# Optimization experiments

Measured on AMD Instinct MI355X. Metric: run time of the kernel, lower is better.

The kernel has to match this reference:

```python
import jax, jax.numpy as jnp
import numpy as np

B, S, H = 4, 2048, 2048
FFN, E, TOP_K = 5632, 8, 2

def setup_inputs() -> dict:
    key = jax.random.key(0)
    k1, k2, k3, k4, k5 = jax.random.split(key, 5)
    return {
        "hidden_states": jax.random.normal(k1, (B, S, H), dtype=jnp.float32),
        "wg": jax.random.normal(k2, (H, E), dtype=jnp.float32) * 0.02,
        "wg_ema": jnp.zeros((H, E), dtype=jnp.float32),
        "fc1_1": jax.random.normal(k3, (E, FFN, H), dtype=jnp.float32) * 0.02,
        "fc1_2": jax.random.normal(k4, (E, FFN, H), dtype=jnp.float32) * 0.02,
        "fc2": jax.random.normal(k5, (E, H, FFN), dtype=jnp.float32) * 0.02,
    }

def reference(hidden_states, wg, wg_ema, fc1_1, fc1_2, fc2):
    b, s, h = hidden_states.shape
    x = hidden_states.reshape(-1, h)  # [T, H]
    # Router: P6TopkCapGate mixes the live gate with its EMA 50/50.
    wg_running = 0.5 * (wg_ema + wg.astype(jnp.float32))
    router_logits = x.astype(jnp.float32) @ wg_running  # [T, E]
    probs = jax.nn.softmax(router_logits, axis=-1)
    top_vals, top_idx = jax.lax.top_k(probs, TOP_K)  # [T, K]
    routing_weights = (top_vals / top_vals.sum(axis=-1, keepdims=True)).astype(x.dtype)
    out = jnp.zeros_like(x)
    n_experts = fc1_1.shape[0]
    for e in range(n_experts):
        # combine weight per token for this expert (0 if not routed here)
        w_e = jnp.sum(routing_weights * (top_idx == e), axis=-1)  # [T]
        h1 = x @ fc1_1[e].T            # [T, FFN]
        h2 = x @ fc1_2[e].T            # [T, FFN]
        y = (jax.nn.silu(h1) * h2) @ fc2[e].T  # [T, H]
        out = out + w_e[:, None] * y
    return out.reshape(b, s, h), router_logits
```

## Files before the change

### kernel.cpp

```cpp
#include <hip/hip_runtime.h>
#include <stdint.h>

#define TT 8192
#define HD 2048
#define FFN 5632
#define NE 8
#define NPK 11264

typedef float f32x4 __attribute__((ext_vector_type(4)));
typedef _Float16 f16x8 __attribute__((ext_vector_type(8)));
typedef unsigned int u32;

#define OFF_WR    0ul
#define OFF_CNT   65536ul
#define OFF_LISTS 66048ul
#define OFF_TOKW  328192ul
#define OFF_ACT   1048576ul
#define OFF_XH    (OFF_ACT + 184549376ul)
#define OFF_WPK   (OFF_XH + 33554432ul)
#define OFF_W3H   OFF_WPK

__device__ __forceinline__ void gl_lds16(const void* g, void* s) {
  __builtin_amdgcn_global_load_lds((const __attribute__((address_space(1))) u32*)g,
                                   (__attribute__((address_space(3))) u32*)s, 16, 0, 0);
}

__device__ __forceinline__ f16x8 cvt8(f32x4 a, f32x4 b) {
  f16x8 r;
  r[0] = (_Float16)a[0]; r[1] = (_Float16)a[1]; r[2] = (_Float16)a[2]; r[3] = (_Float16)a[3];
  r[4] = (_Float16)b[0]; r[5] = (_Float16)b[1]; r[6] = (_Float16)b[2]; r[7] = (_Float16)b[3];
  return r;
}

__global__ __launch_bounds__(256) void k_cvt(const float* __restrict__ in,
                                             _Float16* __restrict__ out, long n8) {
  long i = (long)blockIdx.x * 256 + threadIdx.x;
  const long stride = (long)gridDim.x * 256;
  for (; i < n8; i += stride) {
    f32x4 a = ((const f32x4*)in)[i * 2];
    f32x4 b = ((const f32x4*)in)[i * 2 + 1];
    ((f16x8*)out)[i] = cvt8(a, b);
  }
}

__global__ __launch_bounds__(256) void k_cvtpack(const float* __restrict__ fc11,
                                                 const float* __restrict__ fc12,
                                                 _Float16* __restrict__ wpk) {
  const long total = (long)NE * NPK * 256;
  long i8 = (long)blockIdx.x * 256 + threadIdx.x;
  const long stride = (long)gridDim.x * 256;
  for (; i8 < total; i8 += stride) {
    int k8 = (int)(i8 & 255);
    long qe = i8 >> 8;
    int q = (int)(qe % NPK);
    int e = (int)(qe / NPK);
    int c = q & 127;
    int f = (q >> 7) * 64 + ((c >> 6) & 1) * 32 + ((c >> 4) & 1) * 16 + (c & 15);
    const float* src = ((c >> 5) & 1 ? fc12 : fc11) + ((size_t)e * FFN + f) * HD + k8 * 8;
    f32x4 a = *(const f32x4*)src;
    f32x4 b = *(const f32x4*)(src + 4);
    *(f16x8*)(wpk + qe * HD + (size_t)k8 * 8) = cvt8(a, b);
  }
}

__global__ __launch_bounds__(256) void k_prep(const float* __restrict__ wg,
                                              const float* __restrict__ wge,
                                              float* __restrict__ wr) {
  int i = blockIdx.x * 256 + threadIdx.x;
  if (i < HD * NE) wr[i] = 0.5f * (wge[i] + wg[i]);
}

__global__ __launch_bounds__(256) void k_router(const float* __restrict__ x,
                                                const float* __restrict__ wr,
                                                float* __restrict__ logits,
                                                float* __restrict__ tokw,
                                                int* __restrict__ lists,
                                                int* __restrict__ cnt) {
  const int t = blockIdx.x, tid = threadIdx.x;
  const float* xr = x + (size_t)t * HD;
  float acc[NE];
#pragma unroll
  for (int e = 0; e < NE; ++e) acc[e] = 0.f;
  for (int h = tid; h < HD; h += 256) {
    float xv = xr[h];
    const float* w = wr + h * NE;
#pragma unroll
    for (int e = 0; e < NE; ++e) acc[e] = fmaf(xv, w[e], acc[e]);
  }
#pragma unroll
  for (int e = 0; e < NE; ++e)
#pragma unroll
    for (int off = 32; off; off >>= 1)
      acc[e] += __shfl_xor(acc[e], off, 64);
  __shared__ float red[4][NE];
  int wv = tid >> 6;
  if ((tid & 63) == 0)
    for (int e = 0; e < NE; ++e) red[wv][e] = acc[e];
  __syncthreads();
  if (tid == 0) {
    float l[NE];
#pragma unroll
    for (int e = 0; e < NE; ++e) l[e] = red[0][e] + red[1][e] + red[2][e] + red[3][e];
#pragma unroll
    for (int e = 0; e < NE; ++e) logits[(size_t)t * NE + e] = l[e];
    int i0 = 0;
    for (int e = 1; e < NE; ++e) if (l[e] > l[i0]) i0 = e;
    int i1 = -1;
    for (int e = 0; e < NE; ++e) if (e != i0 && (i1 < 0 || l[e] > l[i1])) i1 = e;
    float p1 = __expf(l[i1] - l[i0]);
    float s = 1.f + p1;
    tokw[t * 2]     = 1.f / s;
    tokw[t * 2 + 1] = p1 / s;
    int q0 = atomicAdd(&cnt[i0], 1);
    lists[i0 * TT + q0] = t * 2;
    int q1 = atomicAdd(&cnt[i1], 1);
    lists[i1 * TT + q1] = t * 2 + 1;
  }
}

__global__ __launch_bounds__(256, 3) void k_ffn1(const _Float16* __restrict__ xh,
                                                 const _Float16* __restrict__ wpk,
                                                 const int* __restrict__ lists,
                                                 const int* __restrict__ cnt,
                                                 _Float16* __restrict__ act) {
  const int bid = blockIdx.x;
  const int xk = bid & 7;
  const int sq = bid >> 3;
  const int slot = sq / 352;
  const int within = sq - slot * 352;
  const int ct = within >> 2;
  const int rt_in = within & 3;
  const int e = slot & 7;
  const int r = ((xk - e) & 7) + ((slot >> 3) << 3);
  const int rt = r * 4 + rt_in;
  const int count = cnt[e];
  if (rt * 128 >= count) return;
  const int tid = threadIdx.x, lane = tid & 63, wv = tid >> 6;

  __shared__ __align__(16) _Float16 As[2][4096];
  __shared__ __align__(16) _Float16 Bs[2][4096];
  __shared__ int row_pair[128];

  if (tid < 128) {
    int rg = rt * 128 + tid;
    row_pair[tid] = (rg < count) ? lists[e * TT + rg] : -1;
  }
  __syncthreads();

  const int lr = lane >> 2;
  const int srow = wv * 32 + lr;
  const int cp = (lane & 3) ^ ((srow >> 1) & 3);
  const int p0 = row_pair[srow], p1 = row_pair[srow + 16];
  const _Float16* gA0 = xh + (size_t)(p0 >= 0 ? (p0 >> 1) : 0) * HD + cp * 8;
  const _Float16* gA1 = xh + (size_t)(p1 >= 0 ? (p1 >> 1) : 0) * HD + cp * 8;
  const _Float16* gB0 = wpk + ((size_t)e * NPK + (size_t)ct * 128 + srow) * HD + cp * 8;
  const _Float16* gB1 = gB0 + (size_t)16 * HD;

  auto stage = [&](int sl, int k0) {
    gl_lds16(gA0 + k0, &As[sl][wv * 1024]);
    gl_lds16(gA1 + k0, &As[sl][wv * 1024 + 512]);
    gl_lds16(gB0 + k0, &Bs[sl][wv * 1024]);
    gl_lds16(gB1 + k0, &Bs[sl][wv * 1024 + 512]);
  };

  const f32x4 z4 = {0.f, 0.f, 0.f, 0.f};
  f32x4 acc[4][4];
#pragma unroll
  for (int m = 0; m < 4; ++m)
#pragma unroll
    for (int n = 0; n < 4; ++n) acc[m][n] = z4;

  const int fr = lane & 15, kq = lane >> 4;
  const int wrow = (wv >> 1) * 64, wcol = (wv & 1) * 64;
  int aoff[4], boff[4];
#pragma unroll
  for (int m = 0; m < 4; ++m) {
    int rr = wrow + m * 16 + fr;
    aoff[m] = rr * 32 + (kq ^ ((rr >> 1) & 3)) * 8;
  }
#pragma unroll
  for (int n = 0; n < 4; ++n) {
    int rr = wcol + n * 16 + fr;
    boff[n] = rr * 32 + (kq ^ ((rr >> 1) & 3)) * 8;
  }

  stage(0, 0);
  __syncthreads();

  const int NS = HD / 32;
  for (int ks = 0; ks < NS; ++ks) {
    const int buf = ks & 1;
    if (ks + 1 < NS) stage(buf ^ 1, (ks + 1) * 32);
    f16x8 fa[4], fb[4];
#pragma unroll
    for (int m = 0; m < 4; ++m) fa[m] = *(const f16x8*)&As[buf][aoff[m]];
#pragma unroll
    for (int n = 0; n < 4; ++n) fb[n] = *(const f16x8*)&Bs[buf][boff[n]];
    __builtin_amdgcn_s_setprio(1);
#pragma unroll
    for (int m = 0; m < 4; ++m)
#pragma unroll
      for (int n = 0; n < 4; ++n)
        acc[m][n] = __builtin_amdgcn_mfma_f32_16x16x32_f16(fa[m], fb[n], acc[m][n], 0, 0, 0);
    __builtin_amdgcn_s_setprio(0);
    __syncthreads();
  }

  const int wn = wv & 1;
  const int rbase = wrow + kq * 4;
#pragma unroll
  for (int m = 0; m < 4; ++m) {
#pragma unroll
    for (int n = 0; n < 2; ++n) {
      const int f = ct * 64 + wn * 32 + n * 16 + fr;
#pragma unroll
      for (int j = 0; j < 4; ++j) {
        int rl = rbase + m * 16 + j;
        int pr = row_pair[rl];
        if (pr >= 0) {
          float h1 = acc[m][n][j], h2 = acc[m][n + 2][j];
          float sv = h1 / (1.f + __expf(-h1));
          act[(size_t)pr * FFN + f] = (_Float16)(sv * h2);
        }
      }
    }
  }
}

__global__ __launch_bounds__(256, 3) void k_ffn2(const _Float16* __restrict__ act,
                                                 const _Float16* __restrict__ w3h,
                                                 const int* __restrict__ lists,
                                                 const int* __restrict__ cnt,
                                                 const float* __restrict__ tokw,
                                                 float* __restrict__ out) {
  const int bid = blockIdx.x;
  const int xk = bid & 7;
  const int sq = bid >> 3;
  const int e = sq >> 7;
  const int within = sq & 127;
  const int rt = within >> 1;
  const int ct = (((xk - e) & 7) << 1) + (within & 1);
  const int count = cnt[e];
  if (rt * 128 >= count) return;
  const int tid = threadIdx.x, lane = tid & 63, wv = tid >> 6;

  __shared__ __align__(16) _Float16 As[2][4096];
  __shared__ __align__(16) _Float16 Bs[2][4096];
  __shared__ int row_pair[128];
  __shared__ float row_w[128];

  if (tid < 128) {
    int rg = rt * 128 + tid;
    int pr = (rg < count) ? lists[e * TT + rg] : -1;
    row_pair[tid] = pr;
    row_w[tid] = (pr >= 0) ? tokw[pr] : 0.f;
  }
  __syncthreads();

  const int lr = lane >> 2;
  const int srow = wv * 32 + lr;
  const int cp = (lane & 3) ^ ((srow >> 1) & 3);
  const int p0 = row_pair[srow], p1 = row_pair[srow + 16];
  const _Float16* gA0 = act + (size_t)(p0 >= 0 ? p0 : 0) * FFN + cp * 8;
  const _Float16* gA1 = act + (size_t)(p1 >= 0 ? p1 : 0) * FFN + cp * 8;
  const _Float16* gB0 = w3h + ((size_t)e * HD + (size_t)ct * 128 + srow) * FFN + cp * 8;
  const _Float16* gB1 = gB0 + (size_t)16 * FFN;

  auto stage = [&](int sl, int k0) {
    gl_lds16(gA0 + k0, &As[sl][wv * 1024]);
    gl_lds16(gA1 + k0, &As[sl][wv * 1024 + 512]);
    gl_lds16(gB0 + k0, &Bs[sl][wv * 1024]);
    gl_lds16(gB1 + k0, &Bs[sl][wv * 1024 + 512]);
  };

  const f32x4 z4 = {0.f, 0.f, 0.f, 0.f};
  f32x4 acc[4][4];
#pragma unroll
  for (int m = 0; m < 4; ++m)
#pragma unroll
    for (int n = 0; n < 4; ++n) acc[m][n] = z4;

  const int fr = lane & 15, kq = lane >> 4;
  const int wrow = (wv >> 1) * 64, wcol = (wv & 1) * 64;
  int aoff[4], boff[4];
#pragma unroll
  for (int m = 0; m < 4; ++m) {
    int rr = wrow + m * 16 + fr;
    aoff[m] = rr * 32 + (kq ^ ((rr >> 1) & 3)) * 8;
  }
#pragma unroll
  for (int n = 0; n < 4; ++n) {
    int rr = wcol + n * 16 + fr;
    boff[n] = rr * 32 + (kq ^ ((rr >> 1) & 3)) * 8;
  }

  stage(0, 0);
  __syncthreads();

  const int NS = FFN / 32;
  for (int ks = 0; ks < NS; ++ks) {
    const int buf = ks & 1;
    if (ks + 1 < NS) stage(buf ^ 1, (ks + 1) * 32);
    f16x8 fa[4], fb[4];
#pragma unroll
    for (int m = 0; m < 4; ++m) fa[m] = *(const f16x8*)&As[buf][aoff[m]];
#pragma unroll
    for (int n = 0; n < 4; ++n) fb[n] = *(const f16x8*)&Bs[buf][boff[n]];
    __builtin_amdgcn_s_setprio(1);
#pragma unroll
    for (int m = 0; m < 4; ++m)
#pragma unroll
      for (int n = 0; n < 4; ++n)
        acc[m][n] = __builtin_amdgcn_mfma_f32_16x16x32_f16(fa[m], fb[n], acc[m][n], 0, 0, 0);
    __builtin_amdgcn_s_setprio(0);
    __syncthreads();
  }

  const int rbase = wrow + kq * 4;
#pragma unroll
  for (int m = 0; m < 4; ++m) {
#pragma unroll
    for (int n = 0; n < 4; ++n) {
      const int col = ct * 128 + wcol + n * 16 + fr;
#pragma unroll
      for (int j = 0; j < 4; ++j) {
        int rl = rbase + m * 16 + j;
        int pr = row_pair[rl];
        if (pr >= 0) {
          float v = acc[m][n][j] * row_w[rl];
          unsafeAtomicAdd(out + (size_t)(pr >> 1) * HD + col, v);
        }
      }
    }
  }
}

extern "C" void kernel_launch(void* const* d_in, const int* in_sizes, int n_in,
                              void* d_out, int out_size, void* d_ws, size_t ws_size,
                              hipStream_t stream) {
  (void)in_sizes; (void)n_in; (void)out_size; (void)ws_size;
  const float* x    = (const float*)d_in[0];
  const float* wg   = (const float*)d_in[1];
  const float* wge  = (const float*)d_in[2];
  const float* fc11 = (const float*)d_in[3];
  const float* fc12 = (const float*)d_in[4];
  const float* fc2  = (const float*)d_in[5];
  float* out    = (float*)d_out;
  float* logits = out + (size_t)TT * HD;

  char* ws = (char*)d_ws;
  float* wr      = (float*)(ws + OFF_WR);
  int*   cnt     = (int*)(ws + OFF_CNT);
  int*   lists   = (int*)(ws + OFF_LISTS);
  float* tokw    = (float*)(ws + OFF_TOKW);
  _Float16* act  = (_Float16*)(ws + OFF_ACT);
  _Float16* xh   = (_Float16*)(ws + OFF_XH);
  _Float16* wpk  = (_Float16*)(ws + OFF_WPK);
  _Float16* w3h  = (_Float16*)(ws + OFF_W3H);

  hipMemsetAsync(out, 0, (size_t)TT * HD * sizeof(float), stream);
  hipMemsetAsync(cnt, 0, NE * sizeof(int), stream);

  k_prep<<<dim3((HD * NE + 255) / 256), 256, 0, stream>>>(wg, wge, wr);
  k_router<<<dim3(TT), 256, 0, stream>>>(x, wr, logits, tokw, lists, cnt);

  k_cvt<<<dim3(2048), 256, 0, stream>>>(x, xh, (long)TT * HD / 8);
  k_cvtpack<<<dim3(2048), 256, 0, stream>>>(fc11, fc12, wpk);

  k_ffn1<<<dim3(64 * 88 * NE), 256, 0, stream>>>(xh, wpk, lists, cnt, act);

  k_cvt<<<dim3(2048), 256, 0, stream>>>(fc2, w3h, (long)NE * HD * FFN / 8);

  k_ffn2<<<dim3(64 * 16 * NE), 256, 0, stream>>>(act, w3h, lists, cnt, tokw, out);
}
```

Measured before the change: 2.193 ms.

## Switch expert GEMMs to 32x32x16 MFMA and fuse x fp16 conversion into router

Both expert GEMM kernels now use 32x32x16 f16 MFMA tiles with 16-wide accumulators in place of 16x16x32 tiles. The LDS fragment offsets, the packed weight interleave, and the epilogue row mapping are rewritten to match the new output layout. The router kernel now also writes the fp16 copy of x, which removes the separate conversion kernel and its extra pass over x. Larger MFMA tiles issue fewer instructions and need fewer LDS fragment reads per FLOP, at the cost of different register pressure and a more intricate epilogue layout.

```diff
diff --git a/kernel.cpp b/kernel.cpp
--- a/kernel.cpp
+++ b/kernel.cpp
@@ -8,6 +8,7 @@
 #define NPK 11264
 
 typedef float f32x4 __attribute__((ext_vector_type(4)));
+typedef float f32x16 __attribute__((ext_vector_type(16)));
 typedef _Float16 f16x8 __attribute__((ext_vector_type(8)));
 typedef unsigned int u32;
 
@@ -55,7 +56,7 @@
     int q = (int)(qe % NPK);
     int e = (int)(qe / NPK);
     int c = q & 127;
-    int f = (q >> 7) * 64 + ((c >> 6) & 1) * 32 + ((c >> 4) & 1) * 16 + (c & 15);
+    int f = (q >> 7) * 64 + ((c >> 6) & 1) * 32 + (c & 31);
     const float* src = ((c >> 5) & 1 ? fc12 : fc11) + ((size_t)e * FFN + f) * HD + k8 * 8;
     f32x4 a = *(const f32x4*)src;
     f32x4 b = *(const f32x4*)(src + 4);
@@ -75,14 +76,17 @@
                                                 float* __restrict__ logits,
                                                 float* __restrict__ tokw,
                                                 int* __restrict__ lists,
-                                                int* __restrict__ cnt) {
+                                                int* __restrict__ cnt,
+                                                _Float16* __restrict__ xh) {
   const int t = blockIdx.x, tid = threadIdx.x;
   const float* xr = x + (size_t)t * HD;
+  _Float16* xo = xh + (size_t)t * HD;
   float acc[NE];
 #pragma unroll
   for (int e = 0; e < NE; ++e) acc[e] = 0.f;
   for (int h = tid; h < HD; h += 256) {
     float xv = xr[h];
+    xo[h] = (_Float16)xv;
     const float* w = wr + h * NE;
 #pragma unroll
     for (int e = 0; e < NE; ++e) acc[e] = fmaf(xv, w[e], acc[e]);
@@ -163,25 +167,32 @@
     gl_lds16(gB1 + k0, &Bs[sl][wv * 1024 + 512]);
   };
 
-  const f32x4 z4 = {0.f, 0.f, 0.f, 0.f};
-  f32x4 acc[4][4];
-#pragma unroll
-  for (int m = 0; m < 4; ++m)
-#pragma unroll
-    for (int n = 0; n < 4; ++n) acc[m][n] = z4;
-
-  const int fr = lane & 15, kq = lane >> 4;
+  f32x16 acc[2][2];
+#pragma unroll
+  for (int mi = 0; mi < 2; ++mi)
+#pragma unroll
+    for (int ni = 0; ni < 2; ++ni) acc[mi][ni] = (f32x16)0.f;
+
+  const int l31 = lane & 31, kq5 = lane >> 5;
   const int wrow = (wv >> 1) * 64, wcol = (wv & 1) * 64;
-  int aoff[4], boff[4];
-#pragma unroll
-  for (int m = 0; m < 4; ++m) {
-    int rr = wrow + m * 16 + fr;
-    aoff[m] = rr * 32 + (kq ^ ((rr >> 1) & 3)) * 8;
-  }
-#pragma unroll
-  for (int n = 0; n < 4; ++n) {
-    int rr = wcol + n * 16 + fr;
-    boff[n] = rr * 32 + (kq ^ ((rr >> 1) & 3)) * 8;
+  int aoff[2][2], boff[2][2];
+#pragma unroll
+  for (int mi = 0; mi < 2; ++mi) {
+    int row = wrow + mi * 32 + l31;
+#pragma unroll
+    for (int kb = 0; kb < 2; ++kb) {
+      int gi = kb * 2 + kq5;
+      aoff[mi][kb] = row * 32 + ((gi ^ ((row >> 1) & 3)) << 3);
+    }
+  }
+#pragma unroll
+  for (int ni = 0; ni < 2; ++ni) {
+    int row = wcol + ni * 32 + l31;
+#pragma unroll
+    for (int kb = 0; kb < 2; ++kb) {
+      int gi = kb * 2 + kq5;
+      boff[ni][kb] = row * 32 + ((gi ^ ((row >> 1) & 3)) << 3);
+    }
   }
 
   stage(0, 0);
@@ -191,37 +202,39 @@
   for (int ks = 0; ks < NS; ++ks) {
     const int buf = ks & 1;
     if (ks + 1 < NS) stage(buf ^ 1, (ks + 1) * 32);
-    f16x8 fa[4], fb[4];
-#pragma unroll
-    for (int m = 0; m < 4; ++m) fa[m] = *(const f16x8*)&As[buf][aoff[m]];
-#pragma unroll
-    for (int n = 0; n < 4; ++n) fb[n] = *(const f16x8*)&Bs[buf][boff[n]];
+    f16x8 fa[2][2], fb[2][2];
+#pragma unroll
+    for (int mi = 0; mi < 2; ++mi)
+#pragma unroll
+      for (int kb = 0; kb < 2; ++kb) fa[mi][kb] = *(const f16x8*)&As[buf][aoff[mi][kb]];
+#pragma unroll
+    for (int ni = 0; ni < 2; ++ni)
+#pragma unroll
+      for (int kb = 0; kb < 2; ++kb) fb[ni][kb] = *(const f16x8*)&Bs[buf][boff[ni][kb]];
     __builtin_amdgcn_s_setprio(1);
 #pragma unroll
-    for (int m = 0; m < 4; ++m)
-#pragma unroll
-      for (int n = 0; n < 4; ++n)
-        acc[m][n] = __builtin_amdgcn_mfma_f32_16x16x32_f16(fa[m], fb[n], acc[m][n], 0, 0, 0);
+    for (int kb = 0; kb < 2; ++kb)
+#pragma unroll
+      for (int mi = 0; mi < 2; ++mi)
+#pragma unroll
+        for (int ni = 0; ni < 2; ++ni)
+          acc[mi][ni] = __builtin_amdgcn_mfma_f32_32x32x16_f16(fa[mi][kb], fb[ni][kb], acc[mi][ni], 0, 0, 0);
     __builtin_amdgcn_s_setprio(0);
     __syncthreads();
   }
 
   const int wn = wv & 1;
-  const int rbase = wrow + kq * 4;
-#pragma unroll
-  for (int m = 0; m < 4; ++m) {
-#pragma unroll
-    for (int n = 0; n < 2; ++n) {
-      const int f = ct * 64 + wn * 32 + n * 16 + fr;
-#pragma unroll
-      for (int j = 0; j < 4; ++j) {
-        int rl = rbase + m * 16 + j;
-        int pr = row_pair[rl];
-        if (pr >= 0) {
-          float h1 = acc[m][n][j], h2 = acc[m][n + 2][j];
-          float sv = h1 / (1.f + __expf(-h1));
-          act[(size_t)pr * FFN + f] = (_Float16)(sv * h2);
-        }
+  const int f = ct * 64 + wn * 32 + l31;
+#pragma unroll
+  for (int mi = 0; mi < 2; ++mi) {
+#pragma unroll
+    for (int rr = 0; rr < 16; ++rr) {
+      int row = wrow + mi * 32 + (rr & 3) + 8 * (rr >> 2) + 4 * kq5;
+      int pr = row_pair[row];
+      if (pr >= 0) {
+        float h1 = acc[mi][0][rr], h2 = acc[mi][1][rr];
+        float sv = h1 / (1.f + __expf(-h1));
+        act[(size_t)pr * FFN + f] = (_Float16)(sv * h2);
       }
     }
   }
@@ -273,25 +286,32 @@
     gl_lds16(gB1 + k0, &Bs[sl][wv * 1024 + 512]);
   };
 
-  const f32x4 z4 = {0.f, 0.f, 0.f, 0.f};
-  f32x4 acc[4][4];
-#pragma unroll
-  for (int m = 0; m < 4; ++m)
-#pragma unroll
-    for (int n = 0; n < 4; ++n) acc[m][n] = z4;
-
-  const int fr = lane & 15, kq = lane >> 4;
+  f32x16 acc[2][2];
+#pragma unroll
+  for (int mi = 0; mi < 2; ++mi)
+#pragma unroll
+    for (int ni = 0; ni < 2; ++ni) acc[mi][ni] = (f32x16)0.f;
+
+  const int l31 = lane & 31, kq5 = lane >> 5;
   const int wrow = (wv >> 1) * 64, wcol = (wv & 1) * 64;
-  int aoff[4], boff[4];
-#pragma unroll
-  for (int m = 0; m < 4; ++m) {
-    int rr = wrow + m * 16 + fr;
-    aoff[m] = rr * 32 + (kq ^ ((rr >> 1) & 3)) * 8;
-  }
-#pragma unroll
-  for (int n = 0; n < 4; ++n) {
-    int rr = wcol + n * 16 + fr;
-    boff[n] = rr * 32 + (kq ^ ((rr >> 1) & 3)) * 8;
+  int aoff[2][2], boff[2][2];
+#pragma unroll
+  for (int mi = 0; mi < 2; ++mi) {
+    int row = wrow + mi * 32 + l31;
+#pragma unroll
+    for (int kb = 0; kb < 2; ++kb) {
+      int gi = kb * 2 + kq5;
+      aoff[mi][kb] = row * 32 + ((gi ^ ((row >> 1) & 3)) << 3);
+    }
+  }
+#pragma unroll
+  for (int ni = 0; ni < 2; ++ni) {
+    int row = wcol + ni * 32 + l31;
+#pragma unroll
+    for (int kb = 0; kb < 2; ++kb) {
+      int gi = kb * 2 + kq5;
+      boff[ni][kb] = row * 32 + ((gi ^ ((row >> 1) & 3)) << 3);
+    }
   }
 
   stage(0, 0);
@@ -301,33 +321,38 @@
   for (int ks = 0; ks < NS; ++ks) {
     const int buf = ks & 1;
     if (ks + 1 < NS) stage(buf ^ 1, (ks + 1) * 32);
-    f16x8 fa[4], fb[4];
-#pragma unroll
-    for (int m = 0; m < 4; ++m) fa[m] = *(const f16x8*)&As[buf][aoff[m]];
-#pragma unroll
-    for (int n = 0; n < 4; ++n) fb[n] = *(const f16x8*)&Bs[buf][boff[n]];
+    f16x8 fa[2][2], fb[2][2];
+#pragma unroll
+    for (int mi = 0; mi < 2; ++mi)
+#pragma unroll
+      for (int kb = 0; kb < 2; ++kb) fa[mi][kb] = *(const f16x8*)&As[buf][aoff[mi][kb]];
+#pragma unroll
+    for (int ni = 0; ni < 2; ++ni)
+#pragma unroll
+      for (int kb = 0; kb < 2; ++kb) fb[ni][kb] = *(const f16x8*)&Bs[buf][boff[ni][kb]];
     __builtin_amdgcn_s_setprio(1);
 #pragma unroll
-    for (int m = 0; m < 4; ++m)
-#pragma unroll
-      for (int n = 0; n < 4; ++n)
-        acc[m][n] = __builtin_amdgcn_mfma_f32_16x16x32_f16(fa[m], fb[n], acc[m][n], 0, 0, 0);
+    for (int kb = 0; kb < 2; ++kb)
+#pragma unroll
+      for (int mi = 0; mi < 2; ++mi)
+#pragma unroll
+        for (int ni = 0; ni < 2; ++ni)
+          acc[mi][ni] = __builtin_amdgcn_mfma_f32_32x32x16_f16(fa[mi][kb], fb[ni][kb], acc[mi][ni], 0, 0, 0);
     __builtin_amdgcn_s_setprio(0);
     __syncthreads();
   }
 
-  const int rbase = wrow + kq * 4;
-#pragma unroll
-  for (int m = 0; m < 4; ++m) {
-#pragma unroll
-    for (int n = 0; n < 4; ++n) {
-      const int col = ct * 128 + wcol + n * 16 + fr;
-#pragma unroll
-      for (int j = 0; j < 4; ++j) {
-        int rl = rbase + m * 16 + j;
-        int pr = row_pair[rl];
+#pragma unroll
+  for (int mi = 0; mi < 2; ++mi) {
+#pragma unroll
+    for (int ni = 0; ni < 2; ++ni) {
+      const int col = ct * 128 + wcol + ni * 32 + l31;
+#pragma unroll
+      for (int rr = 0; rr < 16; ++rr) {
+        int row = wrow + mi * 32 + (rr & 3) + 8 * (rr >> 2) + 4 * kq5;
+        int pr = row_pair[row];
         if (pr >= 0) {
-          float v = acc[m][n][j] * row_w[rl];
+          float v = acc[mi][ni][rr] * row_w[row];
           unsafeAtomicAdd(out + (size_t)(pr >> 1) * HD + col, v);
         }
       }
@@ -362,9 +387,8 @@
   hipMemsetAsync(cnt, 0, NE * sizeof(int), stream);
 
   k_prep<<<dim3((HD * NE + 255) / 256), 256, 0, stream>>>(wg, wge, wr);
-  k_router<<<dim3(TT), 256, 0, stream>>>(x, wr, logits, tokw, lists, cnt);
-
-  k_cvt<<<dim3(2048), 256, 0, stream>>>(x, xh, (long)TT * HD / 8);
+  k_router<<<dim3(TT), 256, 0, stream>>>(x, wr, logits, tokw, lists, cnt, xh);
+
   k_cvtpack<<<dim3(2048), 256, 0, stream>>>(fc11, fc12, wpk);
 
   k_ffn1<<<dim3(64 * 88 * NE), 256, 0, stream>>>(xh, wpk, lists, cnt, act);
```

Result: slower. 2.287 ms (+4.3%).

## Enlarge MoE GEMM row tiles to 192 and fuse x fp16 conversion into router

Applied to the files above, without the earlier changes.

Both expert GEMM kernels move from 128-row to 192-row token tiles, with 6x4 MFMA accumulators per wave and a third A-row stage per wave. Each staged weight tile is then reused across more tokens, cutting the weight traffic per FLOP, and the grid mapping is recomputed to match. Separately, the router writes the fp16 copy of x while it reads x, which removes a standalone conversion kernel and one full pass over x. The larger tiles raise register and LDS use, which may lower occupancy, and they waste more work on the partial last tile of each expert.

```diff
diff --git a/kernel.cpp b/kernel.cpp
--- a/kernel.cpp
+++ b/kernel.cpp
@@ -75,14 +75,17 @@
                                                 float* __restrict__ logits,
                                                 float* __restrict__ tokw,
                                                 int* __restrict__ lists,
-                                                int* __restrict__ cnt) {
+                                                int* __restrict__ cnt,
+                                                _Float16* __restrict__ xh) {
   const int t = blockIdx.x, tid = threadIdx.x;
   const float* xr = x + (size_t)t * HD;
+  _Float16* xo = xh + (size_t)t * HD;
   float acc[NE];
 #pragma unroll
   for (int e = 0; e < NE; ++e) acc[e] = 0.f;
   for (int h = tid; h < HD; h += 256) {
     float xv = xr[h];
+    xo[h] = (_Float16)xv;
     const float* w = wr + h * NE;
 #pragma unroll
     for (int e = 0; e < NE; ++e) acc[e] = fmaf(xv, w[e], acc[e]);
@@ -126,55 +129,59 @@
   const int bid = blockIdx.x;
   const int xk = bid & 7;
   const int sq = bid >> 3;
-  const int slot = sq / 352;
-  const int within = sq - slot * 352;
-  const int ct = within >> 2;
-  const int rt_in = within & 3;
+  const int slot = sq / 264;
+  const int within = sq - slot * 264;
+  const int ct = within / 3;
+  const int rt_in = within - ct * 3;
   const int e = slot & 7;
   const int r = ((xk - e) & 7) + ((slot >> 3) << 3);
-  const int rt = r * 4 + rt_in;
+  const int rt = r * 3 + rt_in;
   const int count = cnt[e];
-  if (rt * 128 >= count) return;
+  if (rt * 192 >= count) return;
   const int tid = threadIdx.x, lane = tid & 63, wv = tid >> 6;
 
-  __shared__ __align__(16) _Float16 As[2][4096];
+  __shared__ __align__(16) _Float16 As[2][6144];
   __shared__ __align__(16) _Float16 Bs[2][4096];
-  __shared__ int row_pair[128];
-
-  if (tid < 128) {
-    int rg = rt * 128 + tid;
+  __shared__ int row_pair[192];
+
+  if (tid < 192) {
+    int rg = rt * 192 + tid;
     row_pair[tid] = (rg < count) ? lists[e * TT + rg] : -1;
   }
   __syncthreads();
 
   const int lr = lane >> 2;
-  const int srow = wv * 32 + lr;
-  const int cp = (lane & 3) ^ ((srow >> 1) & 3);
-  const int p0 = row_pair[srow], p1 = row_pair[srow + 16];
-  const _Float16* gA0 = xh + (size_t)(p0 >= 0 ? (p0 >> 1) : 0) * HD + cp * 8;
-  const _Float16* gA1 = xh + (size_t)(p1 >= 0 ? (p1 >> 1) : 0) * HD + cp * 8;
-  const _Float16* gB0 = wpk + ((size_t)e * NPK + (size_t)ct * 128 + srow) * HD + cp * 8;
+  const int cpA = (lane & 3) ^ (((wv * 48 + lr) >> 1) & 3);
+  const int srowA = wv * 48 + lr;
+  const int pA0 = row_pair[srowA], pA1 = row_pair[srowA + 16], pA2 = row_pair[srowA + 32];
+  const _Float16* gA0 = xh + (size_t)(pA0 >= 0 ? (pA0 >> 1) : 0) * HD + cpA * 8;
+  const _Float16* gA1 = xh + (size_t)(pA1 >= 0 ? (pA1 >> 1) : 0) * HD + cpA * 8;
+  const _Float16* gA2 = xh + (size_t)(pA2 >= 0 ? (pA2 >> 1) : 0) * HD + cpA * 8;
+  const int srowB = wv * 32 + lr;
+  const int cpB = (lane & 3) ^ ((srowB >> 1) & 3);
+  const _Float16* gB0 = wpk + ((size_t)e * NPK + (size_t)ct * 128 + srowB) * HD + cpB * 8;
   const _Float16* gB1 = gB0 + (size_t)16 * HD;
 
   auto stage = [&](int sl, int k0) {
-    gl_lds16(gA0 + k0, &As[sl][wv * 1024]);
-    gl_lds16(gA1 + k0, &As[sl][wv * 1024 + 512]);
+    gl_lds16(gA0 + k0, &As[sl][wv * 1536]);
+    gl_lds16(gA1 + k0, &As[sl][wv * 1536 + 512]);
+    gl_lds16(gA2 + k0, &As[sl][wv * 1536 + 1024]);
     gl_lds16(gB0 + k0, &Bs[sl][wv * 1024]);
     gl_lds16(gB1 + k0, &Bs[sl][wv * 1024 + 512]);
   };
 
   const f32x4 z4 = {0.f, 0.f, 0.f, 0.f};
-  f32x4 acc[4][4];
-#pragma unroll
-  for (int m = 0; m < 4; ++m)
+  f32x4 acc[6][4];
+#pragma unroll
+  for (int m = 0; m < 6; ++m)
 #pragma unroll
     for (int n = 0; n < 4; ++n) acc[m][n] = z4;
 
   const int fr = lane & 15, kq = lane >> 4;
-  const int wrow = (wv >> 1) * 64, wcol = (wv & 1) * 64;
-  int aoff[4], boff[4];
-#pragma unroll
-  for (int m = 0; m < 4; ++m) {
+  const int wrow = (wv >> 1) * 96, wcol = (wv & 1) * 64;
+  int aoff[6], boff[4];
+#pragma unroll
+  for (int m = 0; m < 6; ++m) {
     int rr = wrow + m * 16 + fr;
     aoff[m] = rr * 32 + (kq ^ ((rr >> 1) & 3)) * 8;
   }
@@ -191,14 +198,14 @@
   for (int ks = 0; ks < NS; ++ks) {
     const int buf = ks & 1;
     if (ks + 1 < NS) stage(buf ^ 1, (ks + 1) * 32);
-    f16x8 fa[4], fb[4];
-#pragma unroll
-    for (int m = 0; m < 4; ++m) fa[m] = *(const f16x8*)&As[buf][aoff[m]];
+    f16x8 fa[6], fb[4];
+#pragma unroll
+    for (int m = 0; m < 6; ++m) fa[m] = *(const f16x8*)&As[buf][aoff[m]];
 #pragma unroll
     for (int n = 0; n < 4; ++n) fb[n] = *(const f16x8*)&Bs[buf][boff[n]];
     __builtin_amdgcn_s_setprio(1);
 #pragma unroll
-    for (int m = 0; m < 4; ++m)
+    for (int m = 0; m < 6; ++m)
 #pragma unroll
       for (int n = 0; n < 4; ++n)
         acc[m][n] = __builtin_amdgcn_mfma_f32_16x16x32_f16(fa[m], fb[n], acc[m][n], 0, 0, 0);
@@ -209,7 +216,7 @@
   const int wn = wv & 1;
   const int rbase = wrow + kq * 4;
 #pragma unroll
-  for (int m = 0; m < 4; ++m) {
+  for (int m = 0; m < 6; ++m) {
 #pragma unroll
     for (int n = 0; n < 2; ++n) {
       const int f = ct * 64 + wn * 32 + n * 16 + fr;
@@ -236,21 +243,21 @@
   const int bid = blockIdx.x;
   const int xk = bid & 7;
   const int sq = bid >> 3;
-  const int e = sq >> 7;
-  const int within = sq & 127;
+  const int e = sq / 88;
+  const int within = sq - e * 88;
   const int rt = within >> 1;
   const int ct = (((xk - e) & 7) << 1) + (within & 1);
   const int count = cnt[e];
-  if (rt * 128 >= count) return;
+  if (rt * 192 >= count) return;
   const int tid = threadIdx.x, lane = tid & 63, wv = tid >> 6;
 
-  __shared__ __align__(16) _Float16 As[2][4096];
+  __shared__ __align__(16) _Float16 As[2][6144];
   __shared__ __align__(16) _Float16 Bs[2][4096];
-  __shared__ int row_pair[128];
-  __shared__ float row_w[128];
-
-  if (tid < 128) {
-    int rg = rt * 128 + tid;
+  __shared__ int row_pair[192];
+  __shared__ float row_w[192];
+
+  if (tid < 192) {
+    int rg = rt * 192 + tid;
     int pr = (rg < count) ? lists[e * TT + rg] : -1;
     row_pair[tid] = pr;
     row_w[tid] = (pr >= 0) ? tokw[pr] : 0.f;
@@ -258,33 +265,37 @@
   __syncthreads();
 
   const int lr = lane >> 2;
-  const int srow = wv * 32 + lr;
-  const int cp = (lane & 3) ^ ((srow >> 1) & 3);
-  const int p0 = row_pair[srow], p1 = row_pair[srow + 16];
-  const _Float16* gA0 = act + (size_t)(p0 >= 0 ? p0 : 0) * FFN + cp * 8;
-  const _Float16* gA1 = act + (size_t)(p1 >= 0 ? p1 : 0) * FFN + cp * 8;
-  const _Float16* gB0 = w3h + ((size_t)e * HD + (size_t)ct * 128 + srow) * FFN + cp * 8;
+  const int srowA = wv * 48 + lr;
+  const int cpA = (lane & 3) ^ ((srowA >> 1) & 3);
+  const int pA0 = row_pair[srowA], pA1 = row_pair[srowA + 16], pA2 = row_pair[srowA + 32];
+  const _Float16* gA0 = act + (size_t)(pA0 >= 0 ? pA0 : 0) * FFN + cpA * 8;
+  const _Float16* gA1 = act + (size_t)(pA1 >= 0 ? pA1 : 0) * FFN + cpA * 8;
+  const _Float16* gA2 = act + (size_t)(pA2 >= 0 ? pA2 : 0) * FFN + cpA * 8;
+  const int srowB = wv * 32 + lr;
+  const int cpB = (lane & 3) ^ ((srowB >> 1) & 3);
+  const _Float16* gB0 = w3h + ((size_t)e * HD + (size_t)ct * 128 + srowB) * FFN + cpB * 8;
   const _Float16* gB1 = gB0 + (size_t)16 * FFN;
 
   auto stage = [&](int sl, int k0) {
-    gl_lds16(gA0 + k0, &As[sl][wv * 1024]);
-    gl_lds16(gA1 + k0, &As[sl][wv * 1024 + 512]);
+    gl_lds16(gA0 + k0, &As[sl][wv * 1536]);
+    gl_lds16(gA1 + k0, &As[sl][wv * 1536 + 512]);
+    gl_lds16(gA2 + k0, &As[sl][wv * 1536 + 1024]);
     gl_lds16(gB0 + k0, &Bs[sl][wv * 1024]);
     gl_lds16(gB1 + k0, &Bs[sl][wv * 1024 + 512]);
   };
 
   const f32x4 z4 = {0.f, 0.f, 0.f, 0.f};
-  f32x4 acc[4][4];
-#pragma unroll
-  for (int m = 0; m < 4; ++m)
+  f32x4 acc[6][4];
+#pragma unroll
+  for (int m = 0; m < 6; ++m)
 #pragma unroll
     for (int n = 0; n < 4; ++n) acc[m][n] = z4;
 
   const int fr = lane & 15, kq = lane >> 4;
-  const int wrow = (wv >> 1) * 64, wcol = (wv & 1) * 64;
-  int aoff[4], boff[4];
-#pragma unroll
-  for (int m = 0; m < 4; ++m) {
+  const int wrow = (wv >> 1) * 96, wcol = (wv & 1) * 64;
+  int aoff[6], boff[4];
+#pragma unroll
+  for (int m = 0; m < 6; ++m) {
     int rr = wrow + m * 16 + fr;
     aoff[m] = rr * 32 + (kq ^ ((rr >> 1) & 3)) * 8;
   }
@@ -301,14 +312,14 @@
   for (int ks = 0; ks < NS; ++ks) {
     const int buf = ks & 1;
     if (ks + 1 < NS) stage(buf ^ 1, (ks + 1) * 32);
-    f16x8 fa[4], fb[4];
-#pragma unroll
-    for (int m = 0; m < 4; ++m) fa[m] = *(const f16x8*)&As[buf][aoff[m]];
+    f16x8 fa[6], fb[4];
+#pragma unroll
+    for (int m = 0; m < 6; ++m) fa[m] = *(const f16x8*)&As[buf][aoff[m]];
 #pragma unroll
     for (int n = 0; n < 4; ++n) fb[n] = *(const f16x8*)&Bs[buf][boff[n]];
     __builtin_amdgcn_s_setprio(1);
 #pragma unroll
-    for (int m = 0; m < 4; ++m)
+    for (int m = 0; m < 6; ++m)
 #pragma unroll
       for (int n = 0; n < 4; ++n)
         acc[m][n] = __builtin_amdgcn_mfma_f32_16x16x32_f16(fa[m], fb[n], acc[m][n], 0, 0, 0);
@@ -318,7 +329,7 @@
 
   const int rbase = wrow + kq * 4;
 #pragma unroll
-  for (int m = 0; m < 4; ++m) {
+  for (int m = 0; m < 6; ++m) {
 #pragma unroll
     for (int n = 0; n < 4; ++n) {
       const int col = ct * 128 + wcol + n * 16 + fr;
@@ -362,14 +373,13 @@
   hipMemsetAsync(cnt, 0, NE * sizeof(int), stream);
 
   k_prep<<<dim3((HD * NE + 255) / 256), 256, 0, stream>>>(wg, wge, wr);
-  k_router<<<dim3(TT), 256, 0, stream>>>(x, wr, logits, tokw, lists, cnt);
-
-  k_cvt<<<dim3(2048), 256, 0, stream>>>(x, xh, (long)TT * HD / 8);
+  k_router<<<dim3(TT), 256, 0, stream>>>(x, wr, logits, tokw, lists, cnt, xh);
+
   k_cvtpack<<<dim3(2048), 256, 0, stream>>>(fc11, fc12, wpk);
 
-  k_ffn1<<<dim3(64 * 88 * NE), 256, 0, stream>>>(xh, wpk, lists, cnt, act);
+  k_ffn1<<<dim3(8 * 16 * 264), 256, 0, stream>>>(xh, wpk, lists, cnt, act);
 
   k_cvt<<<dim3(2048), 256, 0, stream>>>(fc2, w3h, (long)NE * HD * FFN / 8);
 
-  k_ffn2<<<dim3(64 * 16 * NE), 256, 0, stream>>>(act, w3h, lists, cnt, tokw, out);
-}
+  k_ffn2<<<dim3(8 * 8 * 88), 256, 0, stream>>>(act, w3h, lists, cnt, tokw, out);
+}
```

Measured after the change: 1.931 ms. 1.14x faster.
